# Kernel tuning notes

Hardware: AMD Instinct MI355X
Metric: run time of the kernel (lower is better)

The kernel has to match this reference:

```python
import jax, jax.numpy as jnp
import numpy as np

B, S, D_IN, D_OUT = 8, 2048, 1024, 1024

def setup_inputs() -> dict:
    key = jax.random.key(0)
    k1, k2, k3, k4 = jax.random.split(key, 4)
    sc = 0.02
    return {
        "x": jax.random.normal(k1, (B, S, D_IN), dtype=jnp.float32),
        "Wq": jax.random.normal(k2, (D_IN, D_OUT), dtype=jnp.float32) * sc,
        "Wk": jax.random.normal(k3, (D_IN, D_OUT), dtype=jnp.float32) * sc,
        "Wv": jax.random.normal(k4, (D_IN, D_OUT), dtype=jnp.float32) * sc,
    }

def reference(x, Wq, Wk, Wv):
    b, n, _ = x.shape
    d_out = Wq.shape[1]
    q = jnp.einsum('bsd,de->bse', x, Wq)   # [b, n, d_out]
    k = jnp.einsum('bsd,de->bse', x, Wk)
    v = jnp.einsum('bsd,de->bse', x, Wv)
    scores = jnp.einsum('bie,bje->bij', q, k)  # [b, n, n]
    # causal mask: positions j > i set to -inf (triu, diagonal=1)
    causal = jnp.triu(jnp.ones((n, n), dtype=bool), k=1)
    scores = jnp.where(causal[None, :, :], -jnp.inf, scores)
    # NOTE: source applies softmax over dim=1 (query axis), scaled by sqrt(d_out)
    weights = jax.nn.softmax(scores / jnp.sqrt(jnp.float32(d_out)), axis=1)
    # dropout is identity in eval mode (p=0)
    return jnp.einsum('bij,bje->bie', weights, v)
```

## Files before the change

### kernel.cpp

```cpp
#include <hip/hip_runtime.h>
#include <hip/hip_bf16.h>


using bf16 = __hip_bfloat16;
typedef __attribute__((ext_vector_type(8))) short short8;
typedef __attribute__((ext_vector_type(4))) float f32x4;

__device__ __forceinline__ float bfbits2f(unsigned short u) {
  return __uint_as_float((unsigned)u << 16);
}

__global__ void cvt_kernel(const float* __restrict__ in, bf16* __restrict__ out) {
  size_t i = ((size_t)blockIdx.x * 256 + threadIdx.x) * 4;
  float4 v = *(const float4*)(in + i);
  alignas(8) bf16 h[4] = {__float2bfloat16(v.x), __float2bfloat16(v.y),
                          __float2bfloat16(v.z), __float2bfloat16(v.w)};
  *(unsigned long long*)(out + i) = *(const unsigned long long*)h;
}

__global__ void wt_kernel(const float* __restrict__ W0, const float* __restrict__ W1,
                          const float* __restrict__ W2, bf16* __restrict__ Wt,
                          float* __restrict__ lbuf) {
  int tid = threadIdx.x;
  if (blockIdx.z == 3) {
    int bid = blockIdx.y * 16 + blockIdx.x;
    if (bid < 64) lbuf[bid * 256 + tid] = 0.f;
    return;
  }
  const float* W = blockIdx.z == 0 ? W0 : blockIdx.z == 1 ? W1 : W2;
  bf16* O = Wt + (size_t)blockIdx.z * 1048576ull;
  __shared__ float t[64][65];
  int n0 = blockIdx.x * 64, k0 = blockIdx.y * 64;
#pragma unroll
  for (int i = 0; i < 4; ++i) {
    int idx = i * 1024 + tid * 4;
    int r = idx >> 6, c = idx & 63;
    float4 v = *(const float4*)(W + (size_t)(k0 + r) * 1024 + n0 + c);
    t[r][c] = v.x; t[r][c + 1] = v.y; t[r][c + 2] = v.z; t[r][c + 3] = v.w;
  }
  __syncthreads();
#pragma unroll
  for (int i = 0; i < 4; ++i) {
    int idx = i * 1024 + tid * 4;
    int r = idx >> 6, c = idx & 63;
    alignas(8) bf16 h[4] = {__float2bfloat16(t[c][r]), __float2bfloat16(t[c + 1][r]),
                            __float2bfloat16(t[c + 2][r]), __float2bfloat16(t[c + 3][r])};
    *(unsigned long long*)(O + (size_t)(n0 + r) * 1024 + k0 + c) = *(const unsigned long long*)h;
  }
}

__global__ void vhat_kernel(const bf16* __restrict__ QKV, const float* __restrict__ l,
                            bf16* __restrict__ Vt) {
  int lb = blockIdx.z;
  const unsigned short* V =
      (const unsigned short*)QKV + ((size_t)lb * 3 + 2) * 2097152ull;
  bf16* O = Vt + (size_t)lb * 2097152ull;
  const float* lc = l + lb * 2048;
  __shared__ float t[64][65];
  __shared__ float rl[64];
  int j0 = blockIdx.x * 64, e0 = blockIdx.y * 64;
  int tid = threadIdx.x;
  if (tid < 64) rl[tid] = 1.0f / lc[j0 + tid];
#pragma unroll
  for (int i = 0; i < 4; ++i) {
    int idx = i * 1024 + tid * 4;
    int r = idx >> 6, c = idx & 63;
    ushort4 u = *(const ushort4*)(V + (size_t)(j0 + r) * 1024 + e0 + c);
    t[r][c] = bfbits2f(u.x); t[r][c + 1] = bfbits2f(u.y);
    t[r][c + 2] = bfbits2f(u.z); t[r][c + 3] = bfbits2f(u.w);
  }
  __syncthreads();
#pragma unroll
  for (int i = 0; i < 4; ++i) {
    int idx = i * 1024 + tid * 4;
    int r = idx >> 6, c = idx & 63;
    alignas(8) bf16 h[4] = {
        __float2bfloat16(t[c][r] * rl[c]), __float2bfloat16(t[c + 1][r] * rl[c + 1]),
        __float2bfloat16(t[c + 2][r] * rl[c + 2]), __float2bfloat16(t[c + 3][r] * rl[c + 3])};
    *(unsigned long long*)(O + (size_t)(e0 + r) * 2048 + j0 + c) = *(const unsigned long long*)h;
  }
}

template <int EPI, bool VARK>
__device__ __forceinline__ void gemm_bt_body(
    const bf16* __restrict__ A, const bf16* __restrict__ B, void* __restrict__ Cv,
    int lda, int ldb, int ldc, int Kin, int zdivA, int zmodB,
    unsigned long long sA, unsigned long long sB, unsigned long long sC,
    float* __restrict__ lptr) {
  const unsigned gx = gridDim.x, gy = gridDim.y;
  const unsigned per_z = gx * gy;
  const unsigned total = per_z * gridDim.z;
  unsigned id = blockIdx.x + gx * (blockIdx.y + gy * blockIdx.z);
  unsigned lid = (id & 7) * (total >> 3) + (id >> 3);
  const unsigned bz = lid / per_z;
  unsigned rem = lid - bz * per_z;
  constexpr unsigned H = 8;
  const unsigned band = rem / (gx * H);
  const unsigned w = rem - band * (gx * H);
  const unsigned bx = w / H;
  const unsigned by_raw = band * H + (w - bx * H);
  const unsigned by = VARK ? (gy - 1 - by_raw) : by_raw;

  if constexpr (EPI == 1) {
    if (bx > by) return;
  }
  const int z = (int)bz;
  A += (unsigned long long)(z / zdivA) * sA;
  B += (unsigned long long)(z % zmodB) * sB;
  const int K = VARK ? (int)(by + 1) * 128 : Kin;

  alignas(16) __shared__ bf16 As[128 * 64];
  alignas(16) __shared__ bf16 Bs[128 * 64];

  const int tid = threadIdx.x, wave = tid >> 6, lane = tid & 63;
  const int m0 = by * 128, n0 = bx * 128;
  const int srow = tid >> 3;
  const int scol_g = ((tid & 7) ^ (srow & 7)) * 8;
  const int scol_l = (tid & 7) * 8;
  const int wm = (wave >> 1) * 64, wn = (wave & 1) * 64;
  const int fm = lane & 15, sw = lane & 7, kg = lane >> 4;

  f32x4 acc[4][4];
#pragma unroll
  for (int mi = 0; mi < 4; ++mi)
#pragma unroll
    for (int ni = 0; ni < 4; ++ni) acc[mi][ni] = (f32x4){0.f, 0.f, 0.f, 0.f};

  const bf16* Arow = A + (size_t)m0 * lda;
  const bf16* Brow = B + (size_t)n0 * ldb;

  for (int k0 = 0; k0 < K; k0 += 64) {
    __syncthreads();
#pragma unroll
    for (int c = 0; c < 4; ++c) {
      int row = c * 32 + srow;
      __builtin_amdgcn_global_load_lds(
          (const __attribute__((address_space(1))) void*)(Arow + (size_t)row * lda + k0 + scol_g),
          (__attribute__((address_space(3))) void*)(As + row * 64 + scol_l), 16, 0, 0);
    }
#pragma unroll
    for (int c = 0; c < 4; ++c) {
      int row = c * 32 + srow;
      __builtin_amdgcn_global_load_lds(
          (const __attribute__((address_space(1))) void*)(Brow + (size_t)row * ldb + k0 + scol_g),
          (__attribute__((address_space(3))) void*)(Bs + row * 64 + scol_l), 16, 0, 0);
    }
    __syncthreads();
#pragma unroll
    for (int ks = 0; ks < 2; ++ks) {
      const int pc = ((ks * 4 + kg) ^ sw) * 8;
      short8 af[4], bf_[4];
#pragma unroll
      for (int i = 0; i < 4; ++i) {
        af[i] = *(const short8*)(As + (wm + i * 16 + fm) * 64 + pc);
        bf_[i] = *(const short8*)(Bs + (wn + i * 16 + fm) * 64 + pc);
      }
#pragma unroll
      for (int mi = 0; mi < 4; ++mi)
#pragma unroll
        for (int ni = 0; ni < 4; ++ni)
          acc[mi][ni] = __builtin_amdgcn_mfma_f32_16x16x32_bf16(af[mi], bf_[ni], acc[mi][ni], 0, 0, 0);
    }
  }

  const int cr = kg * 4, cc = fm;
  if constexpr (EPI == 2) {
    float* C = (float*)Cv + (unsigned long long)z * sC;
#pragma unroll
    for (int mi = 0; mi < 4; ++mi)
#pragma unroll
      for (int ni = 0; ni < 4; ++ni)
#pragma unroll
        for (int r = 0; r < 4; ++r)
          C[(size_t)(m0 + wm + mi * 16 + cr + r) * ldc + (n0 + wn + ni * 16 + cc)] = acc[mi][ni][r];
  } else if constexpr (EPI == 0) {
    bf16* C = (bf16*)Cv + (unsigned long long)z * sC;
#pragma unroll
    for (int mi = 0; mi < 4; ++mi)
#pragma unroll
      for (int ni = 0; ni < 4; ++ni)
#pragma unroll
        for (int r = 0; r < 4; ++r)
          C[(size_t)(m0 + wm + mi * 16 + cr + r) * ldc + (n0 + wn + ni * 16 + cc)] =
              __float2bfloat16(acc[mi][ni][r]);
  } else {
    bf16* C = (bf16*)Cv + (unsigned long long)z * sC;
    float colpart[4] = {0.f, 0.f, 0.f, 0.f};
#pragma unroll
    for (int mi = 0; mi < 4; ++mi)
#pragma unroll
      for (int ni = 0; ni < 4; ++ni)
#pragma unroll
        for (int r = 0; r < 4; ++r) {
          int gm = m0 + wm + mi * 16 + cr + r;
          int gn = n0 + wn + ni * 16 + cc;
          float s = acc[mi][ni][r] * 0.03125f;
          float p = (gn <= gm) ? __expf(s) : 0.f;
          colpart[ni] += p;
          C[(size_t)gm * ldc + gn] = __float2bfloat16(p);
        }
    float* lcol = lptr + (size_t)z * 2048 + n0 + wn;
#pragma unroll
    for (int ni = 0; ni < 4; ++ni) {
      float s = colpart[ni];
      s += __shfl_xor(s, 16);
      s += __shfl_xor(s, 32);
      if (lane < 16) atomicAdd(&lcol[ni * 16 + lane], s);
    }
  }
}

__global__ __launch_bounds__(256, 4) void gemm_qkv(
    const bf16* __restrict__ A, const bf16* __restrict__ B, void* __restrict__ Cv,
    int lda, int ldb, int ldc, int Kin, int zdivA, int zmodB,
    unsigned long long sA, unsigned long long sB, unsigned long long sC) {
  gemm_bt_body<0, false>(A, B, Cv, lda, ldb, ldc, Kin, zdivA, zmodB, sA, sB, sC, nullptr);
}
__global__ __launch_bounds__(256, 4) void gemm_scores(
    const bf16* __restrict__ A, const bf16* __restrict__ B, void* __restrict__ Cv,
    int lda, int ldb, int ldc, int Kin, int zdivA, int zmodB,
    unsigned long long sA, unsigned long long sB, unsigned long long sC,
    float* __restrict__ lptr) {
  gemm_bt_body<1, false>(A, B, Cv, lda, ldb, ldc, Kin, zdivA, zmodB, sA, sB, sC, lptr);
}
__global__ __launch_bounds__(256, 4) void gemm_pv(
    const bf16* __restrict__ A, const bf16* __restrict__ B, void* __restrict__ Cv,
    int lda, int ldb, int ldc, int Kin, int zdivA, int zmodB,
    unsigned long long sA, unsigned long long sB, unsigned long long sC) {
  gemm_bt_body<2, true>(A, B, Cv, lda, ldb, ldc, Kin, zdivA, zmodB, sA, sB, sC, nullptr);
}

extern "C" void kernel_launch(void* const* d_in, const int* in_sizes, int n_in,
                              void* d_out, int out_size, void* d_ws, size_t ws_size,
                              hipStream_t stream) {
  const float* x = (const float*)d_in[0];
  const float* Wq = (const float*)d_in[1];
  const float* Wk = (const float*)d_in[2];
  const float* Wv = (const float*)d_in[3];
  float* out = (float*)d_out;

  constexpr unsigned long long X_EL = 2048ull * 1024;
  constexpr unsigned long long QKV_EL = 3ull * X_EL;
  constexpr unsigned long long P_EL = 2048ull * 2048;
  constexpr unsigned long long VT_EL = 1024ull * 2048;
  constexpr unsigned long long WT_B = 3ull * 1024 * 1024 * 2;
  constexpr unsigned long long LB_B = 8ull * 2048 * 4;
  constexpr unsigned long long PER_B = 2 * (X_EL + QKV_EL + P_EL + VT_EL);

  size_t NB = 1;
  for (size_t nb : {(size_t)8, (size_t)4, (size_t)2})
    if (WT_B + LB_B + nb * PER_B <= ws_size) { NB = nb; break; }

  char* p = (char*)d_ws;
  bf16* Wt = (bf16*)p;   p += WT_B;
  float* lbuf = (float*)p; p += LB_B;
  bf16* Xb = (bf16*)p;   p += 2 * NB * X_EL;
  bf16* QKV = (bf16*)p;  p += 2 * NB * QKV_EL;
  bf16* P = (bf16*)p;    p += 2 * NB * P_EL;
  bf16* Vt = (bf16*)p;

  wt_kernel<<<dim3(16, 16, 4), 256, 0, stream>>>(Wq, Wk, Wv, Wt, lbuf);

  for (size_t b0 = 0; b0 < 8; b0 += NB) {
    cvt_kernel<<<dim3((unsigned)(NB * 2048)), 256, 0, stream>>>(x + b0 * X_EL, Xb);
    gemm_qkv<<<dim3(8, 16, (unsigned)(NB * 3)), 256, 0, stream>>>(
        Xb, Wt, QKV, 1024, 1024, 1024, 1024, 3, 3, X_EL, 1048576ull, X_EL);
    gemm_scores<<<dim3(16, 16, (unsigned)NB), 256, 0, stream>>>(
        QKV, QKV + X_EL, P, 1024, 1024, 2048, 1024, 1, 1 << 30, QKV_EL, QKV_EL, P_EL,
        lbuf + b0 * 2048);
    vhat_kernel<<<dim3(32, 16, (unsigned)NB), 256, 0, stream>>>(QKV, lbuf + b0 * 2048, Vt);
    gemm_pv<<<dim3(8, 16, (unsigned)NB), 256, 0, stream>>>(
        P, Vt, out + b0 * X_EL, 2048, 2048, 1024, 0, 1, 1 << 30, P_EL, VT_EL, X_EL);
  }
}
```

Measured before the change: 334.0 us.

## Replace 128x128 GEMM tiles with 256x256 double-buffered, phase-pipelined 8-wave kernel

Moves all three GEMMs (QKV projection, causal scores, PV) from 128x128 tiles with 4 waves and single-buffered LDS to 256x256 tiles with 8 waves and double-buffered LDS. The K loop is split into four quadrant phases, each issuing the next global-to-LDS load while running MFMAs on the current data, with explicit vmcnt waits, barriers and setprio. This is meant to hide global load latency and raise arithmetic intensity per tile. In exchange, LDS use and register pressure go up and fewer blocks run per CU. The causal scores grid becomes coarser, so more wasted work falls on diagonal tiles.

Measured after the change: 405.0 us. +21.2%, slower.

```diff
diff --git a/kernel.cpp b/kernel.cpp
--- a/kernel.cpp
+++ b/kernel.cpp
@@ -5,6 +5,7 @@
 using bf16 = __hip_bfloat16;
 typedef __attribute__((ext_vector_type(8))) short short8;
 typedef __attribute__((ext_vector_type(4))) float f32x4;
+typedef unsigned long long ull;
 
 __device__ __forceinline__ float bfbits2f(unsigned short u) {
   return __uint_as_float((unsigned)u << 16);
@@ -81,12 +82,57 @@
   }
 }
 
+template <int QA, int QB>
+__device__ __forceinline__ void phase256(
+    bf16 (*As)[256][64], bf16 (*Bs)[256][64], const int buf,
+    f32x4 (&acc)[2][2][4][2], const int wm, const int wn, const int fm, const int kg,
+    const bf16* gsrc, const int gld, bf16* ldst,
+    const int srow, const int scg, const int scl, const bool vm4) {
+  short8 af[2][4], bw[2][2];
+#pragma unroll
+  for (int i = 0; i < 4; ++i) {
+    const int row = QA * 128 + wm * 64 + i * 16 + fm;
+    const int x = row & 7;
+#pragma unroll
+    for (int ks = 0; ks < 2; ++ks)
+      af[ks][i] = *(const short8*)(&As[buf][row][((ks * 4 + kg) ^ x) * 8]);
+  }
+#pragma unroll
+  for (int j = 0; j < 2; ++j) {
+    const int col = QB * 128 + wn * 32 + j * 16 + fm;
+    const int x = col & 7;
+#pragma unroll
+    for (int ks = 0; ks < 2; ++ks)
+      bw[ks][j] = *(const short8*)(&Bs[buf][col][((ks * 4 + kg) ^ x) * 8]);
+  }
+#pragma unroll
+  for (int r = 0; r < 2; ++r)
+    __builtin_amdgcn_global_load_lds(
+        (const __attribute__((address_space(1))) void*)(gsrc + (size_t)(r * 64 + srow) * gld + scg),
+        (__attribute__((address_space(3))) void*)(ldst + (r * 64 + srow) * 64 + scl), 16, 0, 0);
+  __builtin_amdgcn_s_barrier();
+  __builtin_amdgcn_s_setprio(1);
+#pragma unroll
+  for (int ks = 0; ks < 2; ++ks)
+#pragma unroll
+    for (int i = 0; i < 4; ++i)
+#pragma unroll
+      for (int j = 0; j < 2; ++j)
+        acc[QA][QB][i][j] = __builtin_amdgcn_mfma_f32_16x16x32_bf16(
+            af[ks][i], bw[ks][j], acc[QA][QB][i][j], 0, 0, 0);
+  __builtin_amdgcn_s_setprio(0);
+  if (vm4) {
+    asm volatile("s_waitcnt vmcnt(4)" ::: "memory");
+    __builtin_amdgcn_sched_barrier(0);
+  }
+  __builtin_amdgcn_s_barrier();
+}
+
 template <int EPI, bool VARK>
-__device__ __forceinline__ void gemm_bt_body(
+__device__ __forceinline__ void gemm256_body(
     const bf16* __restrict__ A, const bf16* __restrict__ B, void* __restrict__ Cv,
     int lda, int ldb, int ldc, int Kin, int zdivA, int zmodB,
-    unsigned long long sA, unsigned long long sB, unsigned long long sC,
-    float* __restrict__ lptr) {
+    ull sA, ull sB, ull sC, float* __restrict__ lptr) {
   const unsigned gx = gridDim.x, gy = gridDim.y;
   const unsigned per_z = gx * gy;
   const unsigned total = per_z * gridDim.z;
@@ -105,129 +151,151 @@
     if (bx > by) return;
   }
   const int z = (int)bz;
-  A += (unsigned long long)(z / zdivA) * sA;
-  B += (unsigned long long)(z % zmodB) * sB;
-  const int K = VARK ? (int)(by + 1) * 128 : Kin;
-
-  alignas(16) __shared__ bf16 As[128 * 64];
-  alignas(16) __shared__ bf16 Bs[128 * 64];
+  A += (ull)(z / zdivA) * sA;
+  B += (ull)(z % zmodB) * sB;
+  const int K = VARK ? (int)(by + 1) * 256 : Kin;
+  const int NT = K >> 6, NU = NT >> 1;
+
+  alignas(16) __shared__ bf16 As[2][256][64];
+  alignas(16) __shared__ bf16 Bs[2][256][64];
 
   const int tid = threadIdx.x, wave = tid >> 6, lane = tid & 63;
-  const int m0 = by * 128, n0 = bx * 128;
+  const int wm = wave >> 2, wn = wave & 3;
+  const int fm = lane & 15, kg = lane >> 4;
+  const int m0 = (int)by * 256, n0 = (int)bx * 256;
   const int srow = tid >> 3;
-  const int scol_g = ((tid & 7) ^ (srow & 7)) * 8;
-  const int scol_l = (tid & 7) * 8;
-  const int wm = (wave >> 1) * 64, wn = (wave & 1) * 64;
-  const int fm = lane & 15, sw = lane & 7, kg = lane >> 4;
-
-  f32x4 acc[4][4];
-#pragma unroll
-  for (int mi = 0; mi < 4; ++mi)
-#pragma unroll
-    for (int ni = 0; ni < 4; ++ni) acc[mi][ni] = (f32x4){0.f, 0.f, 0.f, 0.f};
-
-  const bf16* Arow = A + (size_t)m0 * lda;
-  const bf16* Brow = B + (size_t)n0 * ldb;
-
-  for (int k0 = 0; k0 < K; k0 += 64) {
-    __syncthreads();
-#pragma unroll
-    for (int c = 0; c < 4; ++c) {
-      int row = c * 32 + srow;
+  const int scg = ((tid & 7) ^ (srow & 7)) * 8;
+  const int scl = (tid & 7) * 8;
+
+  const bf16* A0r = A + (size_t)m0 * lda;
+  const bf16* A1r = A0r + (size_t)128 * lda;
+  const bf16* B0r = B + (size_t)n0 * ldb;
+  const bf16* B1r = B0r + (size_t)128 * ldb;
+
+  f32x4 acc[2][2][4][2];
+#pragma unroll
+  for (int qa = 0; qa < 2; ++qa)
+#pragma unroll
+    for (int qb = 0; qb < 2; ++qb)
+#pragma unroll
+      for (int i = 0; i < 4; ++i)
+#pragma unroll
+        for (int j = 0; j < 2; ++j) acc[qa][qb][i][j] = (f32x4){0.f, 0.f, 0.f, 0.f};
+
+  auto stage = [&](const bf16* g, int gld, bf16* l) {
+#pragma unroll
+    for (int r = 0; r < 2; ++r)
       __builtin_amdgcn_global_load_lds(
-          (const __attribute__((address_space(1))) void*)(Arow + (size_t)row * lda + k0 + scol_g),
-          (__attribute__((address_space(3))) void*)(As + row * 64 + scol_l), 16, 0, 0);
-    }
-#pragma unroll
-    for (int c = 0; c < 4; ++c) {
-      int row = c * 32 + srow;
-      __builtin_amdgcn_global_load_lds(
-          (const __attribute__((address_space(1))) void*)(Brow + (size_t)row * ldb + k0 + scol_g),
-          (__attribute__((address_space(3))) void*)(Bs + row * 64 + scol_l), 16, 0, 0);
-    }
-    __syncthreads();
-#pragma unroll
-    for (int ks = 0; ks < 2; ++ks) {
-      const int pc = ((ks * 4 + kg) ^ sw) * 8;
-      short8 af[4], bf_[4];
-#pragma unroll
-      for (int i = 0; i < 4; ++i) {
-        af[i] = *(const short8*)(As + (wm + i * 16 + fm) * 64 + pc);
-        bf_[i] = *(const short8*)(Bs + (wn + i * 16 + fm) * 64 + pc);
-      }
-#pragma unroll
-      for (int mi = 0; mi < 4; ++mi)
-#pragma unroll
-        for (int ni = 0; ni < 4; ++ni)
-          acc[mi][ni] = __builtin_amdgcn_mfma_f32_16x16x32_bf16(af[mi], bf_[ni], acc[mi][ni], 0, 0, 0);
-    }
+          (const __attribute__((address_space(1))) void*)(g + (size_t)(r * 64 + srow) * gld + scg),
+          (__attribute__((address_space(3))) void*)(l + (r * 64 + srow) * 64 + scl), 16, 0, 0);
+  };
+
+  stage(A0r, lda, &As[0][0][0]);
+  stage(B0r, ldb, &Bs[0][0][0]);
+  stage(A1r, lda, &As[0][128][0]);
+  stage(B1r, ldb, &Bs[0][128][0]);
+  stage(A0r + 64, lda, &As[1][0][0]);
+  stage(B0r + 64, ldb, &Bs[1][0][0]);
+  asm volatile("s_waitcnt vmcnt(4)" ::: "memory");
+  __builtin_amdgcn_sched_barrier(0);
+  __builtin_amdgcn_s_barrier();
+
+  for (int u = 0; u < NU; ++u) {
+    const int t = 2 * u;
+    const int k1 = (t + 1) * 64;
+    const int k2 = (t + 2 < NT ? t + 2 : NT - 1) * 64;
+    const int k3 = (t + 3 < NT ? t + 3 : NT - 1) * 64;
+    phase256<0, 0>(As, Bs, 0, acc, wm, wn, fm, kg, A1r + k1, lda, &As[1][128][0], srow, scg, scl, false);
+    phase256<0, 1>(As, Bs, 0, acc, wm, wn, fm, kg, B1r + k1, ldb, &Bs[1][128][0], srow, scg, scl, false);
+    phase256<1, 0>(As, Bs, 0, acc, wm, wn, fm, kg, A0r + k2, lda, &As[0][0][0],   srow, scg, scl, false);
+    phase256<1, 1>(As, Bs, 0, acc, wm, wn, fm, kg, B0r + k2, ldb, &Bs[0][0][0],   srow, scg, scl, true);
+    phase256<0, 0>(As, Bs, 1, acc, wm, wn, fm, kg, A1r + k2, lda, &As[0][128][0], srow, scg, scl, false);
+    phase256<0, 1>(As, Bs, 1, acc, wm, wn, fm, kg, B1r + k2, ldb, &Bs[0][128][0], srow, scg, scl, false);
+    phase256<1, 0>(As, Bs, 1, acc, wm, wn, fm, kg, A0r + k3, lda, &As[1][0][0],   srow, scg, scl, false);
+    phase256<1, 1>(As, Bs, 1, acc, wm, wn, fm, kg, B0r + k3, ldb, &Bs[1][0][0],   srow, scg, scl, true);
   }
 
   const int cr = kg * 4, cc = fm;
   if constexpr (EPI == 2) {
-    float* C = (float*)Cv + (unsigned long long)z * sC;
-#pragma unroll
-    for (int mi = 0; mi < 4; ++mi)
-#pragma unroll
-      for (int ni = 0; ni < 4; ++ni)
-#pragma unroll
-        for (int r = 0; r < 4; ++r)
-          C[(size_t)(m0 + wm + mi * 16 + cr + r) * ldc + (n0 + wn + ni * 16 + cc)] = acc[mi][ni][r];
+    float* C = (float*)Cv + (ull)z * sC;
+#pragma unroll
+    for (int qa = 0; qa < 2; ++qa)
+#pragma unroll
+      for (int qb = 0; qb < 2; ++qb)
+#pragma unroll
+        for (int i = 0; i < 4; ++i)
+#pragma unroll
+          for (int j = 0; j < 2; ++j)
+#pragma unroll
+            for (int r = 0; r < 4; ++r)
+              C[(size_t)(m0 + qa * 128 + wm * 64 + i * 16 + cr + r) * ldc +
+                (n0 + qb * 128 + wn * 32 + j * 16 + cc)] = acc[qa][qb][i][j][r];
   } else if constexpr (EPI == 0) {
-    bf16* C = (bf16*)Cv + (unsigned long long)z * sC;
-#pragma unroll
-    for (int mi = 0; mi < 4; ++mi)
-#pragma unroll
-      for (int ni = 0; ni < 4; ++ni)
-#pragma unroll
-        for (int r = 0; r < 4; ++r)
-          C[(size_t)(m0 + wm + mi * 16 + cr + r) * ldc + (n0 + wn + ni * 16 + cc)] =
-              __float2bfloat16(acc[mi][ni][r]);
+    bf16* C = (bf16*)Cv + (ull)z * sC;
+#pragma unroll
+    for (int qa = 0; qa < 2; ++qa)
+#pragma unroll
+      for (int qb = 0; qb < 2; ++qb)
+#pragma unroll
+        for (int i = 0; i < 4; ++i)
+#pragma unroll
+          for (int j = 0; j < 2; ++j)
+#pragma unroll
+            for (int r = 0; r < 4; ++r)
+              C[(size_t)(m0 + qa * 128 + wm * 64 + i * 16 + cr + r) * ldc +
+                (n0 + qb * 128 + wn * 32 + j * 16 + cc)] =
+                  __float2bfloat16(acc[qa][qb][i][j][r]);
   } else {
-    bf16* C = (bf16*)Cv + (unsigned long long)z * sC;
-    float colpart[4] = {0.f, 0.f, 0.f, 0.f};
-#pragma unroll
-    for (int mi = 0; mi < 4; ++mi)
-#pragma unroll
-      for (int ni = 0; ni < 4; ++ni)
-#pragma unroll
-        for (int r = 0; r < 4; ++r) {
-          int gm = m0 + wm + mi * 16 + cr + r;
-          int gn = n0 + wn + ni * 16 + cc;
-          float s = acc[mi][ni][r] * 0.03125f;
-          float p = (gn <= gm) ? __expf(s) : 0.f;
-          colpart[ni] += p;
-          C[(size_t)gm * ldc + gn] = __float2bfloat16(p);
-        }
-    float* lcol = lptr + (size_t)z * 2048 + n0 + wn;
-#pragma unroll
-    for (int ni = 0; ni < 4; ++ni) {
-      float s = colpart[ni];
-      s += __shfl_xor(s, 16);
-      s += __shfl_xor(s, 32);
-      if (lane < 16) atomicAdd(&lcol[ni * 16 + lane], s);
-    }
-  }
-}
-
-__global__ __launch_bounds__(256, 4) void gemm_qkv(
+    bf16* C = (bf16*)Cv + (ull)z * sC;
+    float colpart[2][2] = {{0.f, 0.f}, {0.f, 0.f}};
+#pragma unroll
+    for (int qa = 0; qa < 2; ++qa)
+#pragma unroll
+      for (int qb = 0; qb < 2; ++qb)
+#pragma unroll
+        for (int i = 0; i < 4; ++i)
+#pragma unroll
+          for (int j = 0; j < 2; ++j)
+#pragma unroll
+            for (int r = 0; r < 4; ++r) {
+              int gm = m0 + qa * 128 + wm * 64 + i * 16 + cr + r;
+              int gn = n0 + qb * 128 + wn * 32 + j * 16 + cc;
+              float s = acc[qa][qb][i][j][r] * 0.03125f;
+              float p = (gn <= gm) ? __expf(s) : 0.f;
+              colpart[qb][j] += p;
+              C[(size_t)gm * ldc + gn] = __float2bfloat16(p);
+            }
+    float* lbase = lptr + (size_t)z * 2048;
+#pragma unroll
+    for (int qb = 0; qb < 2; ++qb)
+#pragma unroll
+      for (int j = 0; j < 2; ++j) {
+        float s = colpart[qb][j];
+        s += __shfl_xor(s, 16);
+        s += __shfl_xor(s, 32);
+        if (lane < 16)
+          atomicAdd(&lbase[n0 + qb * 128 + wn * 32 + j * 16 + lane], s);
+      }
+  }
+}
+
+__global__ __launch_bounds__(512, 2) void gemm_qkv(
     const bf16* __restrict__ A, const bf16* __restrict__ B, void* __restrict__ Cv,
     int lda, int ldb, int ldc, int Kin, int zdivA, int zmodB,
-    unsigned long long sA, unsigned long long sB, unsigned long long sC) {
-  gemm_bt_body<0, false>(A, B, Cv, lda, ldb, ldc, Kin, zdivA, zmodB, sA, sB, sC, nullptr);
-}
-__global__ __launch_bounds__(256, 4) void gemm_scores(
+    ull sA, ull sB, ull sC) {
+  gemm256_body<0, false>(A, B, Cv, lda, ldb, ldc, Kin, zdivA, zmodB, sA, sB, sC, nullptr);
+}
+__global__ __launch_bounds__(512, 2) void gemm_scores(
     const bf16* __restrict__ A, const bf16* __restrict__ B, void* __restrict__ Cv,
     int lda, int ldb, int ldc, int Kin, int zdivA, int zmodB,
-    unsigned long long sA, unsigned long long sB, unsigned long long sC,
-    float* __restrict__ lptr) {
-  gemm_bt_body<1, false>(A, B, Cv, lda, ldb, ldc, Kin, zdivA, zmodB, sA, sB, sC, lptr);
-}
-__global__ __launch_bounds__(256, 4) void gemm_pv(
+    ull sA, ull sB, ull sC, float* __restrict__ lptr) {
+  gemm256_body<1, false>(A, B, Cv, lda, ldb, ldc, Kin, zdivA, zmodB, sA, sB, sC, lptr);
+}
+__global__ __launch_bounds__(512, 2) void gemm_pv(
     const bf16* __restrict__ A, const bf16* __restrict__ B, void* __restrict__ Cv,
     int lda, int ldb, int ldc, int Kin, int zdivA, int zmodB,
-    unsigned long long sA, unsigned long long sB, unsigned long long sC) {
-  gemm_bt_body<2, true>(A, B, Cv, lda, ldb, ldc, Kin, zdivA, zmodB, sA, sB, sC, nullptr);
+    ull sA, ull sB, ull sC) {
+  gemm256_body<2, true>(A, B, Cv, lda, ldb, ldc, Kin, zdivA, zmodB, sA, sB, sC, nullptr);
 }
 
 extern "C" void kernel_launch(void* const* d_in, const int* in_sizes, int n_in,
@@ -263,13 +331,13 @@
 
   for (size_t b0 = 0; b0 < 8; b0 += NB) {
     cvt_kernel<<<dim3((unsigned)(NB * 2048)), 256, 0, stream>>>(x + b0 * X_EL, Xb);
-    gemm_qkv<<<dim3(8, 16, (unsigned)(NB * 3)), 256, 0, stream>>>(
+    gemm_qkv<<<dim3(4, 8, (unsigned)(NB * 3)), 512, 0, stream>>>(
         Xb, Wt, QKV, 1024, 1024, 1024, 1024, 3, 3, X_EL, 1048576ull, X_EL);
-    gemm_scores<<<dim3(16, 16, (unsigned)NB), 256, 0, stream>>>(
+    gemm_scores<<<dim3(8, 8, (unsigned)NB), 512, 0, stream>>>(
         QKV, QKV + X_EL, P, 1024, 1024, 2048, 1024, 1, 1 << 30, QKV_EL, QKV_EL, P_EL,
         lbuf + b0 * 2048);
     vhat_kernel<<<dim3(32, 16, (unsigned)NB), 256, 0, stream>>>(QKV, lbuf + b0 * 2048, Vt);
-    gemm_pv<<<dim3(8, 16, (unsigned)NB), 256, 0, stream>>>(
+    gemm_pv<<<dim3(4, 8, (unsigned)NB), 512, 0, stream>>>(
         P, Vt, out + b0 * X_EL, 2048, 2048, 1024, 0, 1, 1 << 30, P_EL, VT_EL, X_EL);
   }
 }
```
